# Performance work log

Hardware: AMD Instinct MI355X
Metric: run time of the kernel (lower is better)

Reference implementation:

```python
import jax, jax.numpy as jnp
import numpy as np

N_QUBITS = 8
N_LAYERS = 3
B = 32768
IN_F = 512
OUT_F = 512


def _apply_1q(state, G, q):
    # state: (B, 2,...,2) complex64; G: (2,2) shared or (B,2,2) per-sample gate
    s = jnp.moveaxis(state, 1 + q, -1)
    if G.ndim == 3:
        s = jnp.einsum('bij,...j->...i'.replace('...', 'b...').replace('b...ij', 'bij'), G, s) if False else jnp.einsum('bij,b...j->b...i', G, s)
    else:
        s = jnp.einsum('ij,b...j->b...i', G, s)
    return jnp.moveaxis(s, -1, 1 + q)


def _cnot(state, c, t):
    # flip target axis on the control=1 slice
    ca, ta = 1 + c, 1 + t
    s0 = jax.lax.index_in_dim(state, 0, ca, keepdims=True)
    s1 = jax.lax.index_in_dim(state, 1, ca, keepdims=True)
    s1 = jnp.flip(s1, axis=ta)
    return jnp.concatenate([s0, s1], axis=ca)


def _circuit(angles, qparams):
    # angles: (B, 8) RY embedding angles; qparams: (3, 8) RX layer angles
    b = angles.shape[0]
    state = jnp.zeros((b, 2 ** N_QUBITS), dtype=jnp.complex64).at[:, 0].set(1.0)
    state = state.reshape((b,) + (2,) * N_QUBITS)
    # RY(theta) = [[c, -s], [s, c]], per-sample angles
    half = 0.5 * angles
    c, s = jnp.cos(half), jnp.sin(half)
    for q in range(N_QUBITS):
        G = jnp.stack([jnp.stack([c[:, q], -s[:, q]], -1),
                       jnp.stack([s[:, q], c[:, q]], -1)], -2).astype(jnp.complex64)
        state = _apply_1q(state, G, q)
    # layers: RX(params[l,q]) on each wire, then ring of CNOTs
    hp = 0.5 * qparams
    cp, sp = jnp.cos(hp), jnp.sin(hp)
    for l in range(N_LAYERS):
        for q in range(N_QUBITS):
            # RX(theta) = [[c, -i s], [-i s, c]]
            G = jnp.stack([jnp.stack([cp[l, q] + 0j, -1j * sp[l, q]], -1),
                           jnp.stack([-1j * sp[l, q], cp[l, q] + 0j], -1)], -2).astype(jnp.complex64)
            state = _apply_1q(state, G, q)
        for i in range(N_QUBITS - 1):
            state = _cnot(state, i, i + 1)
        state = _cnot(state, N_QUBITS - 1, 0)
    # <Z_q> = P(bit_q=0) - P(bit_q=1)
    probs = jnp.real(state) ** 2 + jnp.imag(state) ** 2
    zs = []
    for q in range(N_QUBITS):
        p = jnp.moveaxis(probs, 1 + q, 1).reshape(b, 2, -1).sum(-1)
        zs.append(p[:, 0] - p[:, 1])
    return jnp.stack(zs, axis=1)  # (B, 8) float32


def setup_inputs() -> dict:
    key = jax.random.key(0)
    k = jax.random.split(key, 6)
    x = jax.random.normal(k[0], (B, IN_F), dtype=jnp.float32)
    fc_w = jax.random.normal(k[1], (N_QUBITS, IN_F), dtype=jnp.float32) / np.sqrt(IN_F)
    fc_b = jax.random.normal(k[2], (N_QUBITS,), dtype=jnp.float32) * 0.01
    qparams = jax.random.normal(k[3], (N_LAYERS, N_QUBITS), dtype=jnp.float32) * 0.1
    post_w = jax.random.normal(k[4], (OUT_F, N_QUBITS), dtype=jnp.float32) / np.sqrt(N_QUBITS)
    post_b = jax.random.normal(k[5], (OUT_F,), dtype=jnp.float32) * 0.01
    return {"x": x, "fc_w": fc_w, "fc_b": fc_b, "qparams": qparams,
            "post_w": post_w, "post_b": post_b}


def reference(x, fc_w, fc_b, qparams, post_w, post_b):
    xproj = x @ fc_w.T + fc_b            # (B, 8) angles
    z = _circuit(xproj, qparams)          # (B, 8) PauliZ expectations
    return z @ post_w.T + post_b          # (B, OUT_F)
```

## Files before the change

kernel.cpp:

```cpp
#include <hip/hip_runtime.h>

#define BLOCK 512
typedef float v2f __attribute__((ext_vector_type(2)));

__device__ __forceinline__ v2f pk_fma(v2f a, v2f b, v2f c) {
  v2f d;
  asm("v_pk_fma_f32 %0, %1, %2, %3" : "=v"(d) : "v"(a), "v"(b), "v"(c));
  return d;
}
__device__ __forceinline__ v2f pk_mul(v2f a, v2f b) {
  v2f d;
  asm("v_pk_mul_f32 %0, %1, %2" : "=v"(d) : "v"(a), "v"(b));
  return d;
}
__device__ __forceinline__ v2f pk_mul_swap(v2f s, v2f p) {
  v2f d;
  asm("v_pk_mul_f32 %0, %1, %2 op_sel:[0,1] op_sel_hi:[1,0]" : "=v"(d) : "v"(s), "v"(p));
  return d;
}

template<int CTRL>
__device__ __forceinline__ float dpp_f(float v) {
  return __int_as_float(__builtin_amdgcn_mov_dpp(__float_as_int(v), CTRL, 0xF, 0xF, true));
}
template<int MASK>
__device__ __forceinline__ float shx(float v) {
  if constexpr (MASK == 1)      return dpp_f<0xB1>(v);
  else if constexpr (MASK == 2) return dpp_f<0x4E>(v);
  else if constexpr (MASK == 8) return dpp_f<0x128>(v);
  else
    return __int_as_float(__builtin_amdgcn_ds_swizzle(__float_as_int(v), 0x101F));
}

__device__ __forceinline__ int gmap(int b) {
#pragma unroll
  for (int j = 0; j < 7; ++j) b ^= ((b >> (j + 1)) & 1) << j;
  b ^= (b & 1) << 7;
  return b;
}

#define MQ_PACKED 0x99CC66B359AC5632ULL

__device__ __forceinline__ void build_w(const float* th, int u, v2f* wr2, float* wup) {
  float uf[8], vf[8];
#pragma unroll
  for (int q = 0; q < 8; ++q) {
    const float h = 0.5f * th[q];
    const float c_ = __cosf(h), s_ = __sinf(h);
    uf[q] = c_ + s_; vf[q] = c_ - s_;
  }
  v2f P01; P01.x = uf[0]; P01.y = vf[0];
  const float r12[4] = {uf[1] * uf[2], vf[1] * uf[2], uf[1] * vf[2], vf[1] * vf[2]};
#pragma unroll
  for (int k = 0; k < 8; ++k) {
    const float rest = r12[k & 3] * ((k & 4) ? vf[3] : uf[3]);
    v2f rr; rr.x = rest; rr.y = rest;
    wr2[k] = pk_mul(P01, rr);
  }
  const bool b4 = (u & 1), b5 = (u & 2), b6 = (u & 4), b7 = (u & 8);
  const float f4 = b4 ? vf[4] : uf[4], g4 = b4 ? uf[4] : vf[4];
  const float f5 = b5 ? vf[5] : uf[5], g5 = b5 ? uf[5] : vf[5];
  const float f6 = b6 ? vf[6] : uf[6], g6 = b6 ? uf[6] : vf[6];
  const float f7 = b7 ? vf[7] : uf[7], g7 = b7 ? uf[7] : vf[7];
  const float A0 = f4 * f5, A1 = g4 * f5, A2 = f4 * g5, A3 = g4 * g5;
  const float B0 = f6 * f7, B1 = g6 * f7, B2 = f6 * g7, B3 = g6 * g7;
  const float wu = A0 * B0;
  wup[0] = wu * (A3 * B0);
  wup[1] = wu * (A1 * B1);
  wup[2] = wu * (A2 * B2);
  wup[3] = wup[1];
  wup[4] = wu * (A3 * B2);
  wup[5] = wu * (A2 * B1);
  wup[6] = wu * (A0 * B3);
  wup[7] = wu * (A1 * B2);
}

__global__ __launch_bounds__(BLOCK, 4) void qcnn_kernel(
    const float* __restrict__ x,   const float* __restrict__ fcw,
    const float* __restrict__ fcb, const float* __restrict__ qp,
    const float* __restrict__ pw,  const float* __restrict__ pb,
    float* __restrict__ out)
{
  __shared__ float s_fcw[8 * 512];
  __shared__ float s_pwt[8 * 512];
  __shared__ float s_pb[512];
  __shared__ float s_beta[256];
  __shared__ v2f   s_K2[8][8][16];

  const int tid = threadIdx.x;

#pragma unroll
  for (int i = tid; i < 1024; i += BLOCK)
    ((float4*)s_fcw)[i] = ((const float4*)fcw)[i];
#pragma unroll
  for (int i = tid; i < 4096; i += BLOCK)
    s_pwt[i] = pw[(i & 511) * 8 + (i >> 9)];
  if (tid < 128) ((float4*)s_pb)[tid] = ((const float4*)pb)[tid];

  if (tid < 256) {
    const int c = tid;
    const int i1 = gmap(c);
    const int i2 = gmap(i1);
    float ang = 0.f;
#pragma unroll
    for (int q = 0; q < 8; ++q) {
      ang += (((c  >> q) & 1) ? 0.5f : -0.5f) * qp[q];
      ang += (((i1 >> q) & 1) ? 0.5f : -0.5f) * qp[8 + q];
      ang += (((i2 >> q) & 1) ? 0.5f : -0.5f) * qp[16 + q];
    }
    s_beta[c] = ang;
  }
  __syncthreads();

#pragma unroll
  for (int i = tid; i < 2048; i += BLOCK) {
    const int q = i >> 8, c = i & 255;
    const int m = (int)((MQ_PACKED >> (8 * q)) & 0xFF);
    const float kv = __cosf(s_beta[c ^ m] - s_beta[c]) * (1.0f / 256.0f);
    const int uu = c >> 4, rr = c & 15;
    ((float*)s_K2)[((q * 8 + (rr >> 1)) * 16 + uu) * 2 + (rr & 1)] = kv;
  }
  __syncthreads();

  const int wave = tid >> 6;
  const int lane = tid & 63;
  const int u = lane & 15;
  const int g = lane >> 4;

  const int base = blockIdx.x * 64 + wave * 8;
  const int sA = base + g;
  const int sB = base + 4 + g;

  const float* xrA = x + (size_t)sA * 512;
  const float* xrB = x + (size_t)sB * 512;
  v2f accA[8], accB[8];
#pragma unroll
  for (int q = 0; q < 8; ++q) {
    accA[q].x = 0.f; accA[q].y = 0.f;
    accB[q].x = 0.f; accB[q].y = 0.f;
  }
#pragma unroll
  for (int t = 0; t < 8; ++t) {
    const float4 xa = *(const float4*)(xrA + u * 4 + t * 64);
    const float4 xb = *(const float4*)(xrB + u * 4 + t * 64);
    v2f xa01; xa01.x = xa.x; xa01.y = xa.y;
    v2f xa23; xa23.x = xa.z; xa23.y = xa.w;
    v2f xb01; xb01.x = xb.x; xb01.y = xb.y;
    v2f xb23; xb23.x = xb.z; xb23.y = xb.w;
#pragma unroll
    for (int q = 0; q < 8; ++q) {
      const float4 wv = *(const float4*)(s_fcw + q * 512 + u * 4 + t * 64);
      v2f w01; w01.x = wv.x; w01.y = wv.y;
      v2f w23; w23.x = wv.z; w23.y = wv.w;
      accA[q] = pk_fma(xa01, w01, accA[q]);
      accA[q] = pk_fma(xa23, w23, accA[q]);
      accB[q] = pk_fma(xb01, w01, accB[q]);
      accB[q] = pk_fma(xb23, w23, accB[q]);
    }
  }
  float thA[8], thB[8];
#pragma unroll
  for (int q = 0; q < 8; ++q) {
    float aA = accA[q].x + accA[q].y;
    float aB = accB[q].x + accB[q].y;
    aA += shx<1>(aA); aB += shx<1>(aB);
    aA += shx<2>(aA); aB += shx<2>(aB);
    aA += shx<4>(aA); aB += shx<4>(aB);
    aA += shx<8>(aA); aB += shx<8>(aB);
    const float fb = fcb[q];
    thA[q] = aA + fb; thB[q] = aB + fb;
  }

  v2f wA[8], wB[8];
  float wupA[8], wupB[8];
  build_w(thA, u, wA, wupA);
  build_w(thB, u, wB, wupB);

  float zpA[8], zpB[8];
  {
    const v2f* kb = (const v2f*)s_K2 + u;
    {
      v2f aA; aA.x = 0.f; aA.y = 0.f; v2f aB = aA;
#pragma unroll
      for (int k = 0; k < 8; ++k) {
        const v2f kv = kb[0 * 128 + k * 16];
        aA = pk_fma(pk_mul(wA[k], wA[k ^ 1]), kv, aA);
        aB = pk_fma(pk_mul(wB[k], wB[k ^ 1]), kv, aB);
      }
      zpA[0] = (aA.x + aA.y) * wupA[0];
      zpB[0] = (aB.x + aB.y) * wupB[0];
    }
    {
      v2f aA; aA.x = 0.f; aA.y = 0.f; v2f aB = aA;
#pragma unroll
      for (int k = 0; k < 8; ++k) {
        const v2f kv = kb[4 * 128 + k * 16];
        aA = pk_fma(pk_mul_swap(wA[k], wA[k ^ 1]), kv, aA);
        aB = pk_fma(pk_mul_swap(wB[k], wB[k ^ 1]), kv, aB);
      }
      zpA[4] = (aA.x + aA.y) * wupA[4];
      zpB[4] = (aB.x + aB.y) * wupB[4];
    }
    {
      v2f a1A, a5A, a1B, a5B;
      a1A.x = a1A.y = a5A.x = a5A.y = 0.f;
      a1B.x = a1B.y = a5B.x = a5B.y = 0.f;
#pragma unroll
      for (int k = 0; k < 8; ++k) {
        const v2f k1 = kb[1 * 128 + k * 16];
        const v2f k5 = kb[5 * 128 + k * 16];
        const v2f pA = pk_mul(wA[k], wA[k ^ 3]);
        const v2f pB = pk_mul(wB[k], wB[k ^ 3]);
        a1A = pk_fma(pA, k1, a1A); a5A = pk_fma(pA, k5, a5A);
        a1B = pk_fma(pB, k1, a1B); a5B = pk_fma(pB, k5, a5B);
      }
      zpA[1] = (a1A.x + a1A.y) * wupA[1]; zpA[5] = (a5A.x + a5A.y) * wupA[5];
      zpB[1] = (a1B.x + a1B.y) * wupB[1]; zpB[5] = (a5B.x + a5B.y) * wupB[5];
    }
    {
      v2f a2A, a6A, a2B, a6B;
      a2A.x = a2A.y = a6A.x = a6A.y = 0.f;
      a2B.x = a2B.y = a6B.x = a6B.y = 0.f;
#pragma unroll
      for (int k = 0; k < 8; ++k) {
        const v2f k2 = kb[2 * 128 + k * 16];
        const v2f k6 = kb[6 * 128 + k * 16];
        const v2f pA = pk_mul(wA[k], wA[k ^ 6]);
        const v2f pB = pk_mul(wB[k], wB[k ^ 6]);
        a2A = pk_fma(pA, k2, a2A); a6A = pk_fma(pA, k6, a6A);
        a2B = pk_fma(pB, k2, a2B); a6B = pk_fma(pB, k6, a6B);
      }
      zpA[2] = (a2A.x + a2A.y) * wupA[2]; zpA[6] = (a6A.x + a6A.y) * wupA[6];
      zpB[2] = (a2B.x + a2B.y) * wupB[2]; zpB[6] = (a6B.x + a6B.y) * wupB[6];
    }
    {
      v2f a3A, a7A, a3B, a7B;
      a3A.x = a3A.y = a7A.x = a7A.y = 0.f;
      a3B.x = a3B.y = a7B.x = a7B.y = 0.f;
#pragma unroll
      for (int k = 0; k < 8; ++k) {
        const v2f k3 = kb[3 * 128 + k * 16];
        const v2f k7 = kb[7 * 128 + k * 16];
        const v2f pA = pk_mul_swap(wA[k], wA[k ^ 4]);
        const v2f pB = pk_mul_swap(wB[k], wB[k ^ 4]);
        a3A = pk_fma(pA, k3, a3A); a7A = pk_fma(pA, k7, a7A);
        a3B = pk_fma(pB, k3, a3B); a7B = pk_fma(pB, k7, a7B);
      }
      zpA[3] = (a3A.x + a3A.y) * wupA[3]; zpA[7] = (a7A.x + a7A.y) * wupA[7];
      zpB[3] = (a3B.x + a3B.y) * wupB[3]; zpB[7] = (a7B.x + a7B.y) * wupB[7];
    }
  }
#pragma unroll
  for (int q = 0; q < 8; ++q) { zpA[q] += shx<1>(zpA[q]); zpB[q] += shx<1>(zpB[q]); }
#pragma unroll
  for (int q = 0; q < 8; ++q) { zpA[q] += shx<2>(zpA[q]); zpB[q] += shx<2>(zpB[q]); }
#pragma unroll
  for (int q = 0; q < 8; ++q) { zpA[q] += shx<4>(zpA[q]); zpB[q] += shx<4>(zpB[q]); }
#pragma unroll
  for (int q = 0; q < 8; ++q) { zpA[q] += shx<8>(zpA[q]); zpB[q] += shx<8>(zpB[q]); }

  v2f zzA[8], zzB[8];
#pragma unroll
  for (int q = 0; q < 8; ++q) {
    zzA[q].x = zpA[q]; zzA[q].y = zpA[q];
    zzB[q].x = zpB[q]; zzB[q].y = zpB[q];
  }
  float* orA = out + (size_t)sA * 512;
  float* orB = out + (size_t)sB * 512;
#pragma unroll
  for (int tt = 0; tt < 8; ++tt) {
    const int o = u * 4 + tt * 64;
    const float4 pbv = *(const float4*)(s_pb + o);
    v2f rA0; rA0.x = pbv.x; rA0.y = pbv.y;
    v2f rA1; rA1.x = pbv.z; rA1.y = pbv.w;
    v2f rB0 = rA0, rB1 = rA1;
#pragma unroll
    for (int q = 0; q < 8; ++q) {
      const float4 wv = *(const float4*)(s_pwt + q * 512 + o);
      v2f w01; w01.x = wv.x; w01.y = wv.y;
      v2f w23; w23.x = wv.z; w23.y = wv.w;
      rA0 = pk_fma(zzA[q], w01, rA0);
      rA1 = pk_fma(zzA[q], w23, rA1);
      rB0 = pk_fma(zzB[q], w01, rB0);
      rB1 = pk_fma(zzB[q], w23, rB1);
    }
    float4 ovA; ovA.x = rA0.x; ovA.y = rA0.y; ovA.z = rA1.x; ovA.w = rA1.y;
    float4 ovB; ovB.x = rB0.x; ovB.y = rB0.y; ovB.z = rB1.x; ovB.w = rB1.y;
    *(float4*)(orA + o) = ovA;
    *(float4*)(orB + o) = ovB;
  }
}

extern "C" void kernel_launch(void* const* d_in, const int* in_sizes, int n_in,
                              void* d_out, int out_size, void* d_ws, size_t ws_size,
                              hipStream_t stream) {
  const float* x   = (const float*)d_in[0];
  const float* fcw = (const float*)d_in[1];
  const float* fcb = (const float*)d_in[2];
  const float* qp  = (const float*)d_in[3];
  const float* pw  = (const float*)d_in[4];
  const float* pb  = (const float*)d_in[5];
  float* out = (float*)d_out;

  dim3 grid(512), block(BLOCK);
  hipLaunchKernelGGL(qcnn_kernel, grid, block, 0, stream, x, fcw, fcb, qp, pw, pb, out);
}
```

Baseline: 124.6 us.

## Read post weights directly from global and widen K table LDS loads

Drops the per-block shared-memory staging of the transposed post weights and bias. The output projection now reads pw rows and pb straight from global memory, where they should be cache-resident, and packs z values in pairs so each output is a dot product followed by a horizontal add. The K table is re-laid out so each lane fetches float4 instead of float2, halving the LDS load count in the expectation stage. This trims the LDS footprint and prologue work, which may allow more blocks per CU, but adds global/L2 traffic for weights in the hot store loop.

```diff
diff --git a/kernel.cpp b/kernel.cpp
--- a/kernel.cpp
+++ b/kernel.cpp
@@ -75,6 +75,59 @@
   wup[7] = wu * (A1 * B2);
 }
 
+template<int Q, int XOR, bool SWAP>
+__device__ __forceinline__ void dot1(const float4* kb4, const v2f* wA, const v2f* wB,
+                                     float wupA, float wupB, float& zA, float& zB) {
+  v2f aA, aB; aA.x = aA.y = 0.f; aB.x = aB.y = 0.f;
+#pragma unroll
+  for (int k2 = 0; k2 < 4; ++k2) {
+    const float4 kv = kb4[(Q * 4 + k2) * 16];
+    v2f klo; klo.x = kv.x; klo.y = kv.y;
+    v2f khi; khi.x = kv.z; khi.y = kv.w;
+    const int k0 = 2 * k2, k1 = 2 * k2 + 1;
+    v2f pA0 = SWAP ? pk_mul_swap(wA[k0], wA[k0 ^ XOR]) : pk_mul(wA[k0], wA[k0 ^ XOR]);
+    v2f pA1 = SWAP ? pk_mul_swap(wA[k1], wA[k1 ^ XOR]) : pk_mul(wA[k1], wA[k1 ^ XOR]);
+    v2f pB0 = SWAP ? pk_mul_swap(wB[k0], wB[k0 ^ XOR]) : pk_mul(wB[k0], wB[k0 ^ XOR]);
+    v2f pB1 = SWAP ? pk_mul_swap(wB[k1], wB[k1 ^ XOR]) : pk_mul(wB[k1], wB[k1 ^ XOR]);
+    aA = pk_fma(pA0, klo, aA);
+    aA = pk_fma(pA1, khi, aA);
+    aB = pk_fma(pB0, klo, aB);
+    aB = pk_fma(pB1, khi, aB);
+  }
+  zA = (aA.x + aA.y) * wupA;
+  zB = (aB.x + aB.y) * wupB;
+}
+template<int Q1, int Q2, int XOR, bool SWAP>
+__device__ __forceinline__ void dot2(const float4* kb4, const v2f* wA, const v2f* wB,
+                                     float wupA1, float wupA2, float wupB1, float wupB2,
+                                     float& zA1, float& zA2, float& zB1, float& zB2) {
+  v2f a1A, a2A, a1B, a2B;
+  a1A.x = a1A.y = a2A.x = a2A.y = 0.f;
+  a1B.x = a1B.y = a2B.x = a2B.y = 0.f;
+#pragma unroll
+  for (int k2 = 0; k2 < 4; ++k2) {
+    const float4 kv1 = kb4[(Q1 * 4 + k2) * 16];
+    const float4 kv2 = kb4[(Q2 * 4 + k2) * 16];
+    v2f k1lo; k1lo.x = kv1.x; k1lo.y = kv1.y;
+    v2f k1hi; k1hi.x = kv1.z; k1hi.y = kv1.w;
+    v2f k2lo; k2lo.x = kv2.x; k2lo.y = kv2.y;
+    v2f k2hi; k2hi.x = kv2.z; k2hi.y = kv2.w;
+    const int k0 = 2 * k2, k1 = 2 * k2 + 1;
+    v2f pA0 = SWAP ? pk_mul_swap(wA[k0], wA[k0 ^ XOR]) : pk_mul(wA[k0], wA[k0 ^ XOR]);
+    v2f pA1 = SWAP ? pk_mul_swap(wA[k1], wA[k1 ^ XOR]) : pk_mul(wA[k1], wA[k1 ^ XOR]);
+    v2f pB0 = SWAP ? pk_mul_swap(wB[k0], wB[k0 ^ XOR]) : pk_mul(wB[k0], wB[k0 ^ XOR]);
+    v2f pB1 = SWAP ? pk_mul_swap(wB[k1], wB[k1 ^ XOR]) : pk_mul(wB[k1], wB[k1 ^ XOR]);
+    a1A = pk_fma(pA0, k1lo, a1A); a1A = pk_fma(pA1, k1hi, a1A);
+    a2A = pk_fma(pA0, k2lo, a2A); a2A = pk_fma(pA1, k2hi, a2A);
+    a1B = pk_fma(pB0, k1lo, a1B); a1B = pk_fma(pB1, k1hi, a1B);
+    a2B = pk_fma(pB0, k2lo, a2B); a2B = pk_fma(pB1, k2hi, a2B);
+  }
+  zA1 = (a1A.x + a1A.y) * wupA1;
+  zA2 = (a2A.x + a2A.y) * wupA2;
+  zB1 = (a1B.x + a1B.y) * wupB1;
+  zB2 = (a2B.x + a2B.y) * wupB2;
+}
+
 __global__ __launch_bounds__(BLOCK, 4) void qcnn_kernel(
     const float* __restrict__ x,   const float* __restrict__ fcw,
     const float* __restrict__ fcb, const float* __restrict__ qp,
@@ -82,21 +135,13 @@
     float* __restrict__ out)
 {
   __shared__ float s_fcw[8 * 512];
-  __shared__ float s_pwt[8 * 512];
-  __shared__ float s_pb[512];
   __shared__ float s_beta[256];
-  __shared__ v2f   s_K2[8][8][16];
+  __shared__ float s_K3[8][4][16][4];
 
   const int tid = threadIdx.x;
 
-#pragma unroll
   for (int i = tid; i < 1024; i += BLOCK)
     ((float4*)s_fcw)[i] = ((const float4*)fcw)[i];
-#pragma unroll
-  for (int i = tid; i < 4096; i += BLOCK)
-    s_pwt[i] = pw[(i & 511) * 8 + (i >> 9)];
-  if (tid < 128) ((float4*)s_pb)[tid] = ((const float4*)pb)[tid];
-
   if (tid < 256) {
     const int c = tid;
     const int i1 = gmap(c);
@@ -112,13 +157,11 @@
   }
   __syncthreads();
 
-#pragma unroll
   for (int i = tid; i < 2048; i += BLOCK) {
     const int q = i >> 8, c = i & 255;
     const int m = (int)((MQ_PACKED >> (8 * q)) & 0xFF);
     const float kv = __cosf(s_beta[c ^ m] - s_beta[c]) * (1.0f / 256.0f);
-    const int uu = c >> 4, rr = c & 15;
-    ((float*)s_K2)[((q * 8 + (rr >> 1)) * 16 + uu) * 2 + (rr & 1)] = kv;
+    s_K3[q][(c & 15) >> 2][c >> 4][c & 3] = kv;
   }
   __syncthreads();
 
@@ -178,77 +221,15 @@
 
   float zpA[8], zpB[8];
   {
-    const v2f* kb = (const v2f*)s_K2 + u;
-    {
-      v2f aA; aA.x = 0.f; aA.y = 0.f; v2f aB = aA;
-#pragma unroll
-      for (int k = 0; k < 8; ++k) {
-        const v2f kv = kb[0 * 128 + k * 16];
-        aA = pk_fma(pk_mul(wA[k], wA[k ^ 1]), kv, aA);
-        aB = pk_fma(pk_mul(wB[k], wB[k ^ 1]), kv, aB);
-      }
-      zpA[0] = (aA.x + aA.y) * wupA[0];
-      zpB[0] = (aB.x + aB.y) * wupB[0];
-    }
-    {
-      v2f aA; aA.x = 0.f; aA.y = 0.f; v2f aB = aA;
-#pragma unroll
-      for (int k = 0; k < 8; ++k) {
-        const v2f kv = kb[4 * 128 + k * 16];
-        aA = pk_fma(pk_mul_swap(wA[k], wA[k ^ 1]), kv, aA);
-        aB = pk_fma(pk_mul_swap(wB[k], wB[k ^ 1]), kv, aB);
-      }
-      zpA[4] = (aA.x + aA.y) * wupA[4];
-      zpB[4] = (aB.x + aB.y) * wupB[4];
-    }
-    {
-      v2f a1A, a5A, a1B, a5B;
-      a1A.x = a1A.y = a5A.x = a5A.y = 0.f;
-      a1B.x = a1B.y = a5B.x = a5B.y = 0.f;
-#pragma unroll
-      for (int k = 0; k < 8; ++k) {
-        const v2f k1 = kb[1 * 128 + k * 16];
-        const v2f k5 = kb[5 * 128 + k * 16];
-        const v2f pA = pk_mul(wA[k], wA[k ^ 3]);
-        const v2f pB = pk_mul(wB[k], wB[k ^ 3]);
-        a1A = pk_fma(pA, k1, a1A); a5A = pk_fma(pA, k5, a5A);
-        a1B = pk_fma(pB, k1, a1B); a5B = pk_fma(pB, k5, a5B);
-      }
-      zpA[1] = (a1A.x + a1A.y) * wupA[1]; zpA[5] = (a5A.x + a5A.y) * wupA[5];
-      zpB[1] = (a1B.x + a1B.y) * wupB[1]; zpB[5] = (a5B.x + a5B.y) * wupB[5];
-    }
-    {
-      v2f a2A, a6A, a2B, a6B;
-      a2A.x = a2A.y = a6A.x = a6A.y = 0.f;
-      a2B.x = a2B.y = a6B.x = a6B.y = 0.f;
-#pragma unroll
-      for (int k = 0; k < 8; ++k) {
-        const v2f k2 = kb[2 * 128 + k * 16];
-        const v2f k6 = kb[6 * 128 + k * 16];
-        const v2f pA = pk_mul(wA[k], wA[k ^ 6]);
-        const v2f pB = pk_mul(wB[k], wB[k ^ 6]);
-        a2A = pk_fma(pA, k2, a2A); a6A = pk_fma(pA, k6, a6A);
-        a2B = pk_fma(pB, k2, a2B); a6B = pk_fma(pB, k6, a6B);
-      }
-      zpA[2] = (a2A.x + a2A.y) * wupA[2]; zpA[6] = (a6A.x + a6A.y) * wupA[6];
-      zpB[2] = (a2B.x + a2B.y) * wupB[2]; zpB[6] = (a6B.x + a6B.y) * wupB[6];
-    }
-    {
-      v2f a3A, a7A, a3B, a7B;
-      a3A.x = a3A.y = a7A.x = a7A.y = 0.f;
-      a3B.x = a3B.y = a7B.x = a7B.y = 0.f;
-#pragma unroll
-      for (int k = 0; k < 8; ++k) {
-        const v2f k3 = kb[3 * 128 + k * 16];
-        const v2f k7 = kb[7 * 128 + k * 16];
-        const v2f pA = pk_mul_swap(wA[k], wA[k ^ 4]);
-        const v2f pB = pk_mul_swap(wB[k], wB[k ^ 4]);
-        a3A = pk_fma(pA, k3, a3A); a7A = pk_fma(pA, k7, a7A);
-        a3B = pk_fma(pB, k3, a3B); a7B = pk_fma(pB, k7, a7B);
-      }
-      zpA[3] = (a3A.x + a3A.y) * wupA[3]; zpA[7] = (a7A.x + a7A.y) * wupA[7];
-      zpB[3] = (a3B.x + a3B.y) * wupB[3]; zpB[7] = (a7B.x + a7B.y) * wupB[7];
-    }
+    const float4* kb4 = ((const float4*)s_K3) + u;
+    dot1<0, 1, false>(kb4, wA, wB, wupA[0], wupB[0], zpA[0], zpB[0]);
+    dot1<4, 1, true >(kb4, wA, wB, wupA[4], wupB[4], zpA[4], zpB[4]);
+    dot2<1, 5, 3, false>(kb4, wA, wB, wupA[1], wupA[5], wupB[1], wupB[5],
+                         zpA[1], zpA[5], zpB[1], zpB[5]);
+    dot2<2, 6, 6, false>(kb4, wA, wB, wupA[2], wupA[6], wupB[2], wupB[6],
+                         zpA[2], zpA[6], zpB[2], zpB[6]);
+    dot2<3, 7, 4, true >(kb4, wA, wB, wupA[3], wupA[7], wupB[3], wupB[7],
+                         zpA[3], zpA[7], zpB[3], zpB[7]);
   }
 #pragma unroll
   for (int q = 0; q < 8; ++q) { zpA[q] += shx<1>(zpA[q]); zpB[q] += shx<1>(zpB[q]); }
@@ -259,33 +240,40 @@
 #pragma unroll
   for (int q = 0; q < 8; ++q) { zpA[q] += shx<8>(zpA[q]); zpB[q] += shx<8>(zpB[q]); }
 
-  v2f zzA[8], zzB[8];
-#pragma unroll
-  for (int q = 0; q < 8; ++q) {
-    zzA[q].x = zpA[q]; zzA[q].y = zpA[q];
-    zzB[q].x = zpB[q]; zzB[q].y = zpB[q];
-  }
+  v2f zA01, zA23, zA45, zA67, zB01, zB23, zB45, zB67;
+  zA01.x = zpA[0]; zA01.y = zpA[1];  zA23.x = zpA[2]; zA23.y = zpA[3];
+  zA45.x = zpA[4]; zA45.y = zpA[5];  zA67.x = zpA[6]; zA67.y = zpA[7];
+  zB01.x = zpB[0]; zB01.y = zpB[1];  zB23.x = zpB[2]; zB23.y = zpB[3];
+  zB45.x = zpB[4]; zB45.y = zpB[5];  zB67.x = zpB[6]; zB67.y = zpB[7];
   float* orA = out + (size_t)sA * 512;
   float* orB = out + (size_t)sB * 512;
 #pragma unroll
   for (int tt = 0; tt < 8; ++tt) {
     const int o = u * 4 + tt * 64;
-    const float4 pbv = *(const float4*)(s_pb + o);
-    v2f rA0; rA0.x = pbv.x; rA0.y = pbv.y;
-    v2f rA1; rA1.x = pbv.z; rA1.y = pbv.w;
-    v2f rB0 = rA0, rB1 = rA1;
-#pragma unroll
-    for (int q = 0; q < 8; ++q) {
-      const float4 wv = *(const float4*)(s_pwt + q * 512 + o);
-      v2f w01; w01.x = wv.x; w01.y = wv.y;
-      v2f w23; w23.x = wv.z; w23.y = wv.w;
-      rA0 = pk_fma(zzA[q], w01, rA0);
-      rA1 = pk_fma(zzA[q], w23, rA1);
-      rB0 = pk_fma(zzB[q], w01, rB0);
-      rB1 = pk_fma(zzB[q], w23, rB1);
+    const float4 pbv = *(const float4*)(pb + o);
+    float resA[4], resB[4];
+#pragma unroll
+    for (int j = 0; j < 4; ++j) {
+      const float4 wa = *(const float4*)(pw + (o + j) * 8);
+      const float4 wb = *(const float4*)(pw + (o + j) * 8 + 4);
+      v2f w01; w01.x = wa.x; w01.y = wa.y;
+      v2f w23; w23.x = wa.z; w23.y = wa.w;
+      v2f w45; w45.x = wb.x; w45.y = wb.y;
+      v2f w67; w67.x = wb.z; w67.y = wb.w;
+      v2f aA = pk_mul(zA01, w01);
+      aA = pk_fma(zA23, w23, aA);
+      aA = pk_fma(zA45, w45, aA);
+      aA = pk_fma(zA67, w67, aA);
+      v2f aB = pk_mul(zB01, w01);
+      aB = pk_fma(zB23, w23, aB);
+      aB = pk_fma(zB45, w45, aB);
+      aB = pk_fma(zB67, w67, aB);
+      const float pbj = (j == 0) ? pbv.x : (j == 1) ? pbv.y : (j == 2) ? pbv.z : pbv.w;
+      resA[j] = aA.x + aA.y + pbj;
+      resB[j] = aB.x + aB.y + pbj;
     }
-    float4 ovA; ovA.x = rA0.x; ovA.y = rA0.y; ovA.z = rA1.x; ovA.w = rA1.y;
-    float4 ovB; ovB.x = rB0.x; ovB.y = rB0.y; ovB.z = rB1.x; ovB.w = rB1.y;
+    float4 ovA; ovA.x = resA[0]; ovA.y = resA[1]; ovA.z = resA[2]; ovA.w = resA[3];
+    float4 ovB; ovB.x = resB[0]; ovB.y = resB[1]; ovB.z = resB[2]; ovB.w = resB[3];
     *(float4*)(orA + o) = ovA;
     *(float4*)(orB + o) = ovB;
   }
```

New measurement: 142.3 us. +14.2%, slower.
